# Kernel optimization log

Measured on AMD Instinct MI355X. Metric: run time of the kernel, lower is better.

Reference implementation:

```python
import jax, jax.numpy as jnp
import numpy as np

B, NBANDS, NCHAN, NTIME = 32, 9, 64, 4096
M = 32
C = M * NBANDS          # 288 spectral-spatial channels
SF = 4                  # strideFactor
TLEN = 2 * SF - 1       # 7 overlapping temporal windows
E = 2                   # embed_dim
H = 2                   # num_heads (head_dim = 1)
NCLASS = 4
BN_EPS = 1e-5


def _renorm(w, maxnorm):
    # torch.renorm(p=2, dim=0): clamp L2 norm of each dim-0 slice to maxnorm
    norms = jnp.sqrt(jnp.sum(w.reshape(w.shape[0], -1) ** 2, axis=1))
    scale = jnp.minimum(1.0, maxnorm / jnp.maximum(norms, 1e-7))
    return w * scale.reshape((-1,) + (1,) * (w.ndim - 1))


def _pos_embed():
    # get_1d_sincos_pos_embed_from_grid(embed_dim=2, len=7)
    pos = np.arange(TLEN, dtype=np.float32)
    omega = 1.0 / (10000.0 ** (np.arange(E // 2, dtype=np.float32) / (E / 2.0)))
    out = pos[:, None] * omega[None, :]
    return jnp.asarray(np.concatenate([np.sin(out), np.cos(out)], axis=1), jnp.float32)  # [TLEN, E]


def setup_inputs() -> dict:
    key = jax.random.key(0)
    ks = jax.random.split(key, 10)
    s = 0.1
    return {
        "x": jax.random.uniform(ks[0], (B, NBANDS, NCHAN, NTIME), jnp.float32),
        "conv_w": jax.random.normal(ks[1], (C, 1, NCHAN, 1), jnp.float32) * s,
        "conv_b": jax.random.normal(ks[2], (C,), jnp.float32) * s,
        "bn_gamma": jnp.ones((C,), jnp.float32),
        "bn_beta": jnp.zeros((C,), jnp.float32),
        "bn_mean": jnp.zeros((C,), jnp.float32),
        "bn_var": jnp.ones((C,), jnp.float32),
        "in_proj_w": jax.random.normal(ks[3], (C, 3 * E, E), jnp.float32) * s,
        "in_proj_b": jax.random.normal(ks[4], (C, 3 * E), jnp.float32) * s,
        "out_proj_w": jax.random.normal(ks[5], (C, E, E), jnp.float32) * s,
        "out_proj_b": jax.random.normal(ks[6], (C, E), jnp.float32) * s,
        "last_w": jax.random.normal(ks[7], (NCLASS, C * TLEN * E), jnp.float32) * s,
        "last_b": jax.random.normal(ks[8], (NCLASS,), jnp.float32) * s,
    }


def _forward(x, conv_w, conv_b, bn_gamma, bn_beta, bn_mean, bn_var,
             in_proj_w, in_proj_b, out_proj_w, out_proj_b, last_w, last_b):
    # --- SCB: grouped conv (nChan,1) + BatchNorm(eval) + swish ---
    w = _renorm(conv_w, 2.0)
    y = jax.lax.conv_general_dilated(
        x, w, window_strides=(1, 1), padding='VALID',
        dimension_numbers=('NCHW', 'OIHW', 'NCHW'),
        feature_group_count=NBANDS) + conv_b[None, :, None, None]      # [B,C,1,NTIME]
    y = (y - bn_mean[None, :, None, None]) * jax.lax.rsqrt(bn_var + BN_EPS)[None, :, None, None]
    y = y * bn_gamma[None, :, None, None] + bn_beta[None, :, None, None]
    y = y * jax.nn.sigmoid(y)  # swish

    # --- overlapping temporal windows stacked on dim 2 ---
    ts = NTIME // (SF * 2)
    xs = jnp.concatenate([y[:, :, :, i * ts:(i + 2) * ts] for i in range(TLEN)], axis=2)  # [B,C,TLEN,2ts]

    # --- tempo_layer: log-var, RMS/mean shape factor ---
    var = jnp.log(jnp.clip(jnp.var(xs, axis=3, keepdims=True, ddof=1), 1e-6, 1e6))
    mean_ = jnp.mean(xs, axis=3, keepdims=True)
    x_rms = jnp.sqrt(jnp.mean(xs ** 2, axis=3, keepdims=True))
    feat = jnp.concatenate([var, x_rms / mean_], axis=3)               # [B,C,TLEN,E]

    # --- batched per-channel multihead self-attention (replaces C-way loop) ---
    yq = feat + _pos_embed()[None, None]                               # [B,C,T,E]
    qkv = jnp.einsum('bcte,cfe->bctf', yq, in_proj_w) + in_proj_b[None, :, None, :]
    q, k, v = jnp.split(qkv, 3, axis=3)
    hd = E // H
    q = q.reshape(B, C, TLEN, H, hd)
    k = k.reshape(B, C, TLEN, H, hd)
    v = v.reshape(B, C, TLEN, H, hd)
    scores = jnp.einsum('bcthd,bcshd->bchts', q, k) / jnp.sqrt(jnp.float32(hd))
    att = jax.nn.softmax(scores, axis=-1)
    o = jnp.einsum('bchts,bcshd->bcthd', att, v).reshape(B, C, TLEN, E)
    o = jnp.einsum('bcte,cfe->bctf', o, out_proj_w) + out_proj_b[None, :, None, :]

    # --- classifier with weight-norm constraint + log-softmax ---
    flat = o.reshape(B, C * TLEN * E)
    lw = _renorm(last_w, 0.5)
    logits = flat @ lw.T + last_b
    return jax.nn.log_softmax(logits, axis=1)


def reference(x, conv_w, conv_b, bn_gamma, bn_beta, bn_mean, bn_var,
              in_proj_w, in_proj_b, out_proj_w, out_proj_b, last_w, last_b):
    return _forward(x, conv_w, conv_b, bn_gamma, bn_beta, bn_mean, bn_var,
                    in_proj_w, in_proj_b, out_proj_w, out_proj_b, last_w, last_b)
```

## Files before the change

kernel.cpp:

```cpp
#include <hip/hip_runtime.h>
#include <math.h>

#define BB     32
#define NBANDS 9
#define NCHAN  64
#define NTIME  4096
#define CC     288
#define TLEN   7
#define NSEG   8
#define SEGLEN 512
#define NCLASS 4

#define WS_WF    0
#define WS_BIAS  (WS_WF + CC*NCHAN)
#define WS_S1    (WS_BIAS + CC)
#define WS_S2    (WS_S1 + BB*CC*NSEG)
#define WS_FLAT  (WS_S2 + BB*CC*NSEG)

typedef _Float16 f16;
typedef __attribute__((ext_vector_type(8))) _Float16 f16x8;
typedef __attribute__((ext_vector_type(4))) float floatx4;

#define IBLK 260
#define BUFF (16 * IBLK)

__device__ __forceinline__ void gl_lds16(const float* g, float* l) {
  __builtin_amdgcn_global_load_lds(
      (const __attribute__((address_space(1))) void*)g,
      (__attribute__((address_space(3))) void*)l, 16, 0, 0);
}

__global__ __launch_bounds__(64) void k0_fold(
    const float* __restrict__ cw, const float* __restrict__ cb,
    const float* __restrict__ gam, const float* __restrict__ bet,
    const float* __restrict__ mu, const float* __restrict__ var,
    f16* __restrict__ Wh, f16* __restrict__ Wl, float* __restrict__ biasf) {
  int c = blockIdx.x;
  int h = threadIdx.x;
  int g = c >> 5, cc = c & 31;
  float w = cw[c * NCHAN + h];
  float sq = w * w;
#pragma unroll
  for (int off = 32; off; off >>= 1) sq += __shfl_down(sq, off, 64);
  sq = __shfl(sq, 0, 64);
  float norm = sqrtf(sq);
  float scale = fminf(1.0f, 2.0f / fmaxf(norm, 1e-7f));
  float bns = gam[c] / sqrtf(var[c] + 1e-5f);
  float wf = w * scale * bns;
  f16 hi = (f16)wf;
  f16 lo = (f16)(wf - (float)hi);
  int o = g * (NCHAN * 32) + h * 32 + cc;
  Wh[o] = hi;
  Wl[o] = lo;
  if (h == 0) biasf[c] = (cb[c] - mu[c]) * bns + bet[c];
}

__global__ __launch_bounds__(256, 4) void k1_conv(
    const float* __restrict__ x, const f16* __restrict__ Wh,
    const f16* __restrict__ Wl, const float* __restrict__ biasf,
    float* __restrict__ S1, float* __restrict__ S2) {
  __shared__ float lds[2][BUFF];
  __shared__ float part[2][32][4];

  int gid = blockIdx.x;
  int seg = gid & 7;
  int g = (gid >> 3) % NBANDS;
  int b = gid / (NBANDS * NSEG);
  int tid = threadIdx.x;
  int w = tid >> 6, lane = tid & 63;
  int quad = lane >> 4, li = lane & 15;

  const float* xp = x + (size_t)(b * NBANDS + g) * NCHAN * NTIME + seg * SEGLEN;
  const f16* whp = Wh + g * (NCHAN * 32);
  const f16* wlp = Wl + g * (NCHAN * 32);

  f16x8 ah[2][2], al[2][2];
#pragma unroll
  for (int mt = 0; mt < 2; ++mt)
#pragma unroll
    for (int kb = 0; kb < 2; ++kb)
#pragma unroll
      for (int j = 0; j < 8; ++j) {
        int idx = (kb * 32 + quad * 8 + j) * 32 + mt * 16 + li;
        ah[mt][kb][j] = whp[idx];
        al[mt][kb][j] = wlp[idx];
      }

  float biasr[2][4];
#pragma unroll
  for (int mt = 0; mt < 2; ++mt)
#pragma unroll
    for (int r = 0; r < 4; ++r)
      biasr[mt][r] = biasf[g * 32 + mt * 16 + quad * 4 + r];

  float s1a[2][4], s2a[2][4];
#pragma unroll
  for (int mt = 0; mt < 2; ++mt)
#pragma unroll
    for (int r = 0; r < 4; ++r) { s1a[mt][r] = 0.0f; s2a[mt][r] = 0.0f; }

#pragma unroll
  for (int i = 0; i < 4; ++i) {
    int I = w * 4 + i;
    gl_lds16(xp + (size_t)(I * 4 + quad) * NTIME + li * 4, &lds[0][I * IBLK]);
  }

#pragma unroll 1
  for (int p = 0; p < 8; ++p) {
    int cur = p & 1;
    if (p < 7) {
#pragma unroll
      for (int i = 0; i < 4; ++i) {
        int I = w * 4 + i;
        gl_lds16(xp + (size_t)(I * 4 + quad) * NTIME + (p + 1) * 64 + li * 4,
                 &lds[cur ^ 1][I * IBLK]);
      }
      asm volatile("s_waitcnt vmcnt(4)" ::: "memory");
    } else {
      asm volatile("s_waitcnt vmcnt(0)" ::: "memory");
    }
    __syncthreads();

    const float* Lb = lds[cur];
    floatx4 acc0 = {0.0f, 0.0f, 0.0f, 0.0f};
    floatx4 acc1 = {0.0f, 0.0f, 0.0f, 0.0f};
#pragma unroll
    for (int kb = 0; kb < 2; ++kb) {
      f16x8 bh, bl;
#pragma unroll
      for (int j = 0; j < 8; ++j) {
        int I = kb * 8 + quad * 2 + (j >> 2);
        int idx = I * IBLK + (j & 3) * 64 + w * 16 + (li >> 2) * 4 + (li & 3);
        float v = Lb[idx];
        f16 hi = (f16)v;
        bh[j] = hi;
        bl[j] = (f16)(v - (float)hi);
      }
      acc0 = __builtin_amdgcn_mfma_f32_16x16x32_f16(ah[0][kb], bh, acc0, 0, 0, 0);
      acc0 = __builtin_amdgcn_mfma_f32_16x16x32_f16(ah[0][kb], bl, acc0, 0, 0, 0);
      acc0 = __builtin_amdgcn_mfma_f32_16x16x32_f16(al[0][kb], bh, acc0, 0, 0, 0);
      acc1 = __builtin_amdgcn_mfma_f32_16x16x32_f16(ah[1][kb], bh, acc1, 0, 0, 0);
      acc1 = __builtin_amdgcn_mfma_f32_16x16x32_f16(ah[1][kb], bl, acc1, 0, 0, 0);
      acc1 = __builtin_amdgcn_mfma_f32_16x16x32_f16(al[1][kb], bh, acc1, 0, 0, 0);
    }
#pragma unroll
    for (int r = 0; r < 4; ++r) {
      float d0 = acc0[r] + biasr[0][r];
      float d1 = acc1[r] + biasr[1][r];
      float y0 = d0 * __builtin_amdgcn_rcpf(1.0f + __expf(-d0));
      float y1 = d1 * __builtin_amdgcn_rcpf(1.0f + __expf(-d1));
      s1a[0][r] += y0; s2a[0][r] = fmaf(y0, y0, s2a[0][r]);
      s1a[1][r] += y1; s2a[1][r] = fmaf(y1, y1, s2a[1][r]);
    }
    __syncthreads();
  }

#pragma unroll
  for (int off = 8; off; off >>= 1) {
#pragma unroll
    for (int mt = 0; mt < 2; ++mt)
#pragma unroll
      for (int r = 0; r < 4; ++r) {
        s1a[mt][r] += __shfl_down(s1a[mt][r], off, 16);
        s2a[mt][r] += __shfl_down(s2a[mt][r], off, 16);
      }
  }

  if (li == 0) {
#pragma unroll
    for (int mt = 0; mt < 2; ++mt)
#pragma unroll
      for (int r = 0; r < 4; ++r) {
        int c = mt * 16 + quad * 4 + r;
        part[0][c][w] = s1a[mt][r];
        part[1][c][w] = s2a[mt][r];
      }
  }
  __syncthreads();
  if (tid < 64) {
    int c = tid >> 1, which = tid & 1;
    float v = part[which][c][0] + part[which][c][1] +
              part[which][c][2] + part[which][c][3];
    size_t o = (size_t)((b * CC) + g * 32 + c) * NSEG + seg;
    if (which == 0) S1[o] = v; else S2[o] = v;
  }
}

__global__ __launch_bounds__(256) void k2_attn(
    const float* __restrict__ S1, const float* __restrict__ S2,
    const float* __restrict__ ipw, const float* __restrict__ ipb,
    const float* __restrict__ opw, const float* __restrict__ opb,
    float* __restrict__ flat) {
  const float PSIN[TLEN] = {0.0f, 0.8414709848f, 0.9092974268f, 0.1411200081f,
                            -0.7568024953f, -0.9589242747f, -0.2794154982f};
  const float PCOS[TLEN] = {1.0f, 0.5403023059f, -0.4161468365f, -0.9899924966f,
                            -0.6536436209f, 0.2836621855f, 0.9601702867f};
  int idx = blockIdx.x * blockDim.x + threadIdx.x;
  if (idx >= BB * CC) return;
  int b = idx / CC, c = idx % CC;
  const float* s1 = S1 + (size_t)(b * CC + c) * NSEG;
  const float* s2 = S2 + (size_t)(b * CC + c) * NSEG;

  float yq[TLEN][2];
#pragma unroll
  for (int t = 0; t < TLEN; ++t) {
    float S1w = s1[t] + s1[t + 1];
    float S2w = s2[t] + s2[t + 1];
    float mean = S1w * (1.0f / 1024.0f);
    float var = (S2w - S1w * S1w * (1.0f / 1024.0f)) * (1.0f / 1023.0f);
    var = fminf(fmaxf(var, 1e-6f), 1e6f);
    float rms = sqrtf(S2w * (1.0f / 1024.0f));
    yq[t][0] = __logf(var) + PSIN[t];
    yq[t][1] = rms / mean + PCOS[t];
  }

  const float* W = ipw + c * 12;
  const float* Bp = ipb + c * 6;
  float q[TLEN][2], k[TLEN][2], v[TLEN][2];
#pragma unroll
  for (int t = 0; t < TLEN; ++t) {
#pragma unroll
    for (int f = 0; f < 6; ++f) {
      float val = W[f * 2 + 0] * yq[t][0] + W[f * 2 + 1] * yq[t][1] + Bp[f];
      if (f < 2) q[t][f] = val;
      else if (f < 4) k[t][f - 2] = val;
      else v[t][f - 4] = val;
    }
  }

  float o[TLEN][2];
#pragma unroll
  for (int h = 0; h < 2; ++h) {
#pragma unroll
    for (int t = 0; t < TLEN; ++t) {
      float sc[TLEN];
      float m = -1e30f;
#pragma unroll
      for (int s = 0; s < TLEN; ++s) {
        sc[s] = q[t][h] * k[s][h];
        m = fmaxf(m, sc[s]);
      }
      float sum = 0.0f, acc = 0.0f;
#pragma unroll
      for (int s = 0; s < TLEN; ++s) {
        float e = __expf(sc[s] - m);
        sum += e;
        acc += e * v[s][h];
      }
      o[t][h] = acc / sum;
    }
  }

  const float* Wo = opw + c * 4;
  const float* Bo = opb + c * 2;
  float* out = flat + (size_t)b * (CC * TLEN * 2) + c * (TLEN * 2);
#pragma unroll
  for (int t = 0; t < TLEN; ++t) {
    out[t * 2 + 0] = Wo[0] * o[t][0] + Wo[1] * o[t][1] + Bo[0];
    out[t * 2 + 1] = Wo[2] * o[t][0] + Wo[3] * o[t][1] + Bo[1];
  }
}

__global__ __launch_bounds__(256) void k3_cls(
    const float* __restrict__ flat, const float* __restrict__ lw,
    const float* __restrict__ lb, float* __restrict__ out) {
  const int FEAT = CC * TLEN * 2;
  int b = blockIdx.x;
  int tid = threadIdx.x;
  const float* f = flat + (size_t)b * FEAT;
  float d[NCLASS] = {0, 0, 0, 0}, n2[NCLASS] = {0, 0, 0, 0};
  for (int j = tid; j < FEAT; j += 256) {
    float fv = f[j];
#pragma unroll
    for (int n = 0; n < NCLASS; ++n) {
      float w = lw[n * FEAT + j];
      d[n] = fmaf(fv, w, d[n]);
      n2[n] = fmaf(w, w, n2[n]);
    }
  }
  __shared__ float red[4][8];
  int lane = tid & 63, wave = tid >> 6;
#pragma unroll
  for (int n = 0; n < NCLASS; ++n) {
#pragma unroll
    for (int off = 32; off; off >>= 1) {
      d[n] += __shfl_down(d[n], off, 64);
      n2[n] += __shfl_down(n2[n], off, 64);
    }
  }
  if (lane == 0) {
#pragma unroll
    for (int n = 0; n < NCLASS; ++n) {
      red[wave][n] = d[n];
      red[wave][n + 4] = n2[n];
    }
  }
  __syncthreads();
  if (tid == 0) {
    float logit[NCLASS];
#pragma unroll
    for (int n = 0; n < NCLASS; ++n) {
      float dn = red[0][n] + red[1][n] + red[2][n] + red[3][n];
      float nn = red[0][n + 4] + red[1][n + 4] + red[2][n + 4] + red[3][n + 4];
      float norm = sqrtf(nn);
      float scale = fminf(1.0f, 0.5f / fmaxf(norm, 1e-7f));
      logit[n] = dn * scale + lb[n];
    }
    float m = fmaxf(fmaxf(logit[0], logit[1]), fmaxf(logit[2], logit[3]));
    float s = 0.0f;
#pragma unroll
    for (int n = 0; n < NCLASS; ++n) s += expf(logit[n] - m);
    float ls = logf(s);
#pragma unroll
    for (int n = 0; n < NCLASS; ++n) out[b * NCLASS + n] = logit[n] - m - ls;
  }
}

extern "C" void kernel_launch(void* const* d_in, const int* in_sizes, int n_in,
                              void* d_out, int out_size, void* d_ws, size_t ws_size,
                              hipStream_t stream) {
  const float* x     = (const float*)d_in[0];
  const float* cw    = (const float*)d_in[1];
  const float* cb    = (const float*)d_in[2];
  const float* gam   = (const float*)d_in[3];
  const float* bet   = (const float*)d_in[4];
  const float* mu    = (const float*)d_in[5];
  const float* var   = (const float*)d_in[6];
  const float* ipw   = (const float*)d_in[7];
  const float* ipb   = (const float*)d_in[8];
  const float* opw   = (const float*)d_in[9];
  const float* opb   = (const float*)d_in[10];
  const float* lw    = (const float*)d_in[11];
  const float* lb    = (const float*)d_in[12];
  float* out = (float*)d_out;

  float* ws = (float*)d_ws;
  f16* Wh = (f16*)(ws + WS_WF);
  f16* Wl = Wh + CC * NCHAN;
  float* biasf = ws + WS_BIAS;
  float* S1    = ws + WS_S1;
  float* S2    = ws + WS_S2;
  float* flat  = ws + WS_FLAT;

  k0_fold<<<CC, 64, 0, stream>>>(cw, cb, gam, bet, mu, var, Wh, Wl, biasf);
  k1_conv<<<BB * NBANDS * NSEG, 256, 0, stream>>>(x, Wh, Wl, biasf, S1, S2);
  k2_attn<<<(BB * CC + 255) / 256, 256, 0, stream>>>(S1, S2, ipw, ipb, opw, opb, flat);
  k3_cls<<<BB, 256, 0, stream>>>(flat, lw, lb, out);
}
```

Baseline: 439.2 us.

## Restructure conv tile loads into 1KB contiguous rows with K-split single buffer

```diff
diff --git a/kernel.cpp b/kernel.cpp
--- a/kernel.cpp
+++ b/kernel.cpp
@@ -20,9 +20,6 @@
 typedef _Float16 f16;
 typedef __attribute__((ext_vector_type(8))) _Float16 f16x8;
 typedef __attribute__((ext_vector_type(4))) float floatx4;
-
-#define IBLK 260
-#define BUFF (16 * IBLK)
 
 __device__ __forceinline__ void gl_lds16(const float* g, float* l) {
   __builtin_amdgcn_global_load_lds(
@@ -55,11 +52,11 @@
   if (h == 0) biasf[c] = (cb[c] - mu[c]) * bns + bet[c];
 }
 
-__global__ __launch_bounds__(256, 4) void k1_conv(
+__global__ __launch_bounds__(256, 3) void k1_conv(
     const float* __restrict__ x, const f16* __restrict__ Wh,
     const f16* __restrict__ Wl, const float* __restrict__ biasf,
     float* __restrict__ S1, float* __restrict__ S2) {
-  __shared__ float lds[2][BUFF];
+  __shared__ float lds[32 * 256];
   __shared__ float part[2][32][4];
 
   int gid = blockIdx.x;
@@ -99,60 +96,59 @@
 #pragma unroll
     for (int r = 0; r < 4; ++r) { s1a[mt][r] = 0.0f; s2a[mt][r] = 0.0f; }
 
-#pragma unroll
-  for (int i = 0; i < 4; ++i) {
-    int I = w * 4 + i;
-    gl_lds16(xp + (size_t)(I * 4 + quad) * NTIME + li * 4, &lds[0][I * IBLK]);
-  }
-
 #pragma unroll 1
-  for (int p = 0; p < 8; ++p) {
-    int cur = p & 1;
-    if (p < 7) {
-#pragma unroll
-      for (int i = 0; i < 4; ++i) {
-        int I = w * 4 + i;
-        gl_lds16(xp + (size_t)(I * 4 + quad) * NTIME + (p + 1) * 64 + li * 4,
-                 &lds[cur ^ 1][I * IBLK]);
-      }
-      asm volatile("s_waitcnt vmcnt(4)" ::: "memory");
-    } else {
+  for (int sp = 0; sp < 2; ++sp) {
+    floatx4 acc0[4], acc1[4];
+#pragma unroll
+    for (int ti = 0; ti < 4; ++ti) {
+      acc0[ti] = (floatx4){0.0f, 0.0f, 0.0f, 0.0f};
+      acc1[ti] = (floatx4){0.0f, 0.0f, 0.0f, 0.0f};
+    }
+
+#pragma unroll 1
+    for (int half = 0; half < 2; ++half) {
+#pragma unroll
+      for (int i = 0; i < 8; ++i) {
+        int lr = w * 8 + i;
+        gl_lds16(xp + (size_t)(half * 32 + lr) * NTIME + sp * 256 + lane * 4,
+                 &lds[lr * 256]);
+      }
       asm volatile("s_waitcnt vmcnt(0)" ::: "memory");
-    }
-    __syncthreads();
-
-    const float* Lb = lds[cur];
-    floatx4 acc0 = {0.0f, 0.0f, 0.0f, 0.0f};
-    floatx4 acc1 = {0.0f, 0.0f, 0.0f, 0.0f};
-#pragma unroll
-    for (int kb = 0; kb < 2; ++kb) {
-      f16x8 bh, bl;
-#pragma unroll
-      for (int j = 0; j < 8; ++j) {
-        int I = kb * 8 + quad * 2 + (j >> 2);
-        int idx = I * IBLK + (j & 3) * 64 + w * 16 + (li >> 2) * 4 + (li & 3);
-        float v = Lb[idx];
-        f16 hi = (f16)v;
-        bh[j] = hi;
-        bl[j] = (f16)(v - (float)hi);
-      }
-      acc0 = __builtin_amdgcn_mfma_f32_16x16x32_f16(ah[0][kb], bh, acc0, 0, 0, 0);
-      acc0 = __builtin_amdgcn_mfma_f32_16x16x32_f16(ah[0][kb], bl, acc0, 0, 0, 0);
-      acc0 = __builtin_amdgcn_mfma_f32_16x16x32_f16(al[0][kb], bh, acc0, 0, 0, 0);
-      acc1 = __builtin_amdgcn_mfma_f32_16x16x32_f16(ah[1][kb], bh, acc1, 0, 0, 0);
-      acc1 = __builtin_amdgcn_mfma_f32_16x16x32_f16(ah[1][kb], bl, acc1, 0, 0, 0);
-      acc1 = __builtin_amdgcn_mfma_f32_16x16x32_f16(al[1][kb], bh, acc1, 0, 0, 0);
-    }
-#pragma unroll
-    for (int r = 0; r < 4; ++r) {
-      float d0 = acc0[r] + biasr[0][r];
-      float d1 = acc1[r] + biasr[1][r];
-      float y0 = d0 * __builtin_amdgcn_rcpf(1.0f + __expf(-d0));
-      float y1 = d1 * __builtin_amdgcn_rcpf(1.0f + __expf(-d1));
-      s1a[0][r] += y0; s2a[0][r] = fmaf(y0, y0, s2a[0][r]);
-      s1a[1][r] += y1; s2a[1][r] = fmaf(y1, y1, s2a[1][r]);
-    }
-    __syncthreads();
+      __syncthreads();
+
+#pragma unroll
+      for (int ti = 0; ti < 4; ++ti) {
+        int tb = (w * 4 + ti) * 16 + li;
+        f16x8 bh, bl;
+#pragma unroll
+        for (int j = 0; j < 8; ++j) {
+          float v = lds[(quad * 8 + j) * 256 + tb];
+          f16 hi = (f16)v;
+          bh[j] = hi;
+          bl[j] = (f16)(v - (float)hi);
+        }
+        acc0[ti] = __builtin_amdgcn_mfma_f32_16x16x32_f16(ah[0][half], bh, acc0[ti], 0, 0, 0);
+        acc0[ti] = __builtin_amdgcn_mfma_f32_16x16x32_f16(ah[0][half], bl, acc0[ti], 0, 0, 0);
+        acc0[ti] = __builtin_amdgcn_mfma_f32_16x16x32_f16(al[0][half], bh, acc0[ti], 0, 0, 0);
+        acc1[ti] = __builtin_amdgcn_mfma_f32_16x16x32_f16(ah[1][half], bh, acc1[ti], 0, 0, 0);
+        acc1[ti] = __builtin_amdgcn_mfma_f32_16x16x32_f16(ah[1][half], bl, acc1[ti], 0, 0, 0);
+        acc1[ti] = __builtin_amdgcn_mfma_f32_16x16x32_f16(al[1][half], bh, acc1[ti], 0, 0, 0);
+      }
+      __syncthreads();
+    }
+
+#pragma unroll
+    for (int ti = 0; ti < 4; ++ti) {
+#pragma unroll
+      for (int r = 0; r < 4; ++r) {
+        float d0 = acc0[ti][r] + biasr[0][r];
+        float d1 = acc1[ti][r] + biasr[1][r];
+        float y0 = d0 * __builtin_amdgcn_rcpf(1.0f + __expf(-d0));
+        float y1 = d1 * __builtin_amdgcn_rcpf(1.0f + __expf(-d1));
+        s1a[0][r] += y0; s2a[0][r] = fmaf(y0, y0, s2a[0][r]);
+        s1a[1][r] += y1; s2a[1][r] = fmaf(y1, y1, s2a[1][r]);
+      }
+    }
   }
 
 #pragma unroll
```

New measurement: 446.7 us. No clear change (+1.7%).
